# Kernel tuning notes

Measured on AMD Instinct MI355X. Metric: run time of the kernel, lower is better.

The kernel has to match this reference:

```python
import jax, jax.numpy as jnp
import numpy as np

N_BLADES = 8
D_BLADE = 128
D_FFN = 512
LN_EPS = 1e-5


def _build_cayley_signs():
    """Cl(3,0) Cayley table: blades indexed by bitmask over {e1,e2,e3}.
    signs[i, j, k] = s where blade_i * blade_j = s * blade_k (Euclidean metric)."""
    def reorder_sign(a, b):
        a >>= 1
        total = 0
        while a:
            total += bin(a & b).count('1')
            a >>= 1
        return 1.0 if total % 2 == 0 else -1.0
    signs = np.zeros((8, 8, 8), dtype=np.float32)
    for i in range(8):
        for j in range(8):
            signs[i, j, i ^ j] = reorder_sign(i, j)
    return jnp.asarray(signs)


def setup_inputs() -> dict:
    key = jax.random.key(0)
    k_x, k_g, k_u, k_d = jax.random.split(key, 4)
    B, T = 4, 4096
    x = jax.random.normal(k_x, (B, T, N_BLADES, D_BLADE), dtype=jnp.float32)
    return {
        'x': x,
        'interaction_weights': jnp.full((N_BLADES, N_BLADES), 0.1, dtype=jnp.float32),
        'geo_gate': jnp.asarray(0.5, dtype=jnp.float32),
        'ln_w': jnp.ones((D_BLADE,), dtype=jnp.float32),
        'ln_b': jnp.zeros((D_BLADE,), dtype=jnp.float32),
        'w_gate': jax.random.normal(k_g, (D_FFN, D_BLADE), dtype=jnp.float32) * 0.02,
        'w_up': jax.random.normal(k_u, (D_FFN, D_BLADE), dtype=jnp.float32) * 0.02,
        'w_down': jax.random.normal(k_d, (D_BLADE, D_FFN), dtype=jnp.float32) * 0.02,
        'cayley_signs': _build_cayley_signs(),
    }


def reference(x, interaction_weights, geo_gate, ln_w, ln_b, w_gate, w_up, w_down, cayley_signs):
    # --- full geometric self-product via Cayley table ---
    w = jax.nn.sigmoid(interaction_weights)              # (i, j)
    signed = cayley_signs * w[:, :, None]                # (i, j, k): fold weights into sign tensor
    # result[b,t,k,d] = sum_ij signed[i,j,k] * x[b,t,i,d] * x[b,t,j,d]
    geo = jnp.einsum('btid,btjd,ijk->btkd', x, x, signed)
    # --- residual gate between geometric product and input ---
    gate = jax.nn.sigmoid(geo_gate)
    mixed = gate * geo + (1.0 - gate) * x                # (B, T, N, D)
    # --- per-blade LayerNorm over d_blade ---
    mu = jnp.mean(mixed, axis=-1, keepdims=True)
    var = jnp.mean(jnp.square(mixed - mu), axis=-1, keepdims=True)
    normed = (mixed - mu) * jax.lax.rsqrt(var + LN_EPS) * ln_w + ln_b
    # --- SwiGLU FFN (no biases) ---
    g = jnp.einsum('btnd,fd->btnf', normed, w_gate)
    u = jnp.einsum('btnd,fd->btnf', normed, w_up)
    h = jax.nn.silu(g) * u
    out = jnp.einsum('btnf,df->btnd', h, w_down)
    return x + out
```

## Files before the change

### kernel.cpp

```cpp
#include <hip/hip_runtime.h>
#include <hip/hip_bf16.h>

typedef unsigned short ushort_t;
typedef __bf16 bf16_t;
typedef bf16_t bf16x8 __attribute__((ext_vector_type(8)));
typedef unsigned short u16x8v __attribute__((ext_vector_type(8)));
typedef float f32x4 __attribute__((ext_vector_type(4)));
typedef unsigned uint32x2 __attribute__((ext_vector_type(2)));
typedef unsigned uint32x4 __attribute__((ext_vector_type(4)));

#define D 128
#define NB 8
#define DFFN 512
#define LN_EPS 1e-5f

#define BARRIER_LGKM() asm volatile("s_waitcnt lgkmcnt(0)\n\ts_barrier" ::: "memory")
#define BARRIER_VM()   asm volatile("s_waitcnt vmcnt(0) lgkmcnt(0)\n\ts_barrier" ::: "memory")
#define PIN(v) asm volatile("" : "+v"(v))

__device__ __forceinline__ ushort_t bf16_rne(float f) {
  union { float f; unsigned u; } c; c.f = f;
  unsigned u = c.u;
  unsigned r = (u + 0x7FFFu + ((u >> 16) & 1u)) >> 16;
  return (ushort_t)r;
}

__device__ __forceinline__ unsigned cvt_pk_bf16(float lo, float hi) {
  unsigned r;
  asm("v_cvt_pk_bf16_f32 %0, %1, %2" : "=v"(r) : "v"(lo), "v"(hi));
  return r;
}

__device__ __forceinline__ bf16x8 loadfrag_bf(const ushort_t* p) {
  u16x8v v = *(const u16x8v*)p;
  return __builtin_bit_cast(bf16x8, v);
}

__device__ __forceinline__ bf16x8 load8_cvt(const float* p) {
  f32x4 a = *(const f32x4*)p;
  f32x4 b = *(const f32x4*)(p + 4);
  u16x8v r;
  r[0] = bf16_rne(a[0]); r[1] = bf16_rne(a[1]);
  r[2] = bf16_rne(a[2]); r[3] = bf16_rne(a[3]);
  r[4] = bf16_rne(b[0]); r[5] = bf16_rne(b[1]);
  r[6] = bf16_rne(b[2]); r[7] = bf16_rne(b[3]);
  return __builtin_bit_cast(bf16x8, r);
}

__device__ __forceinline__ f32x4 mfma16(bf16x8 a, bf16x8 b, f32x4 c) {
  return __builtin_amdgcn_mfma_f32_16x16x32_bf16(a, b, c, 0, 0, 0);
}

__device__ __forceinline__ float readlane_f(float v, int lane) {
  return __builtin_bit_cast(float, __builtin_amdgcn_readlane(__builtin_bit_cast(int, v), lane));
}

__device__ __forceinline__ float fast_rcp(float x) {
  return __builtin_amdgcn_rcpf(x);
}

typedef const __attribute__((address_space(1))) void gv_t;
typedef __attribute__((address_space(3))) void lv_t;
__device__ __forceinline__ void gload_lds16(const void* g, void* l) {
  __builtin_amdgcn_global_load_lds((gv_t*)g, (lv_t*)l, 16, 0, 0);
}

__global__ void cvt_weights(const float* __restrict__ wg,
                            const float* __restrict__ wu,
                            const float* __restrict__ wd,
                            ushort_t* __restrict__ o) {
  int i = blockIdx.x * 256 + threadIdx.x;
  const int n1 = DFFN * D;
  float v;
  if (i < n1)            v = wg[i];
  else if (i < 2 * n1)   v = wu[i - n1];
  else                   v = wd[i - 2 * n1];
  o[i] = bf16_rne(v);
}

__global__ __launch_bounds__(256)
void geo_ln(const float* __restrict__ x,
            const float* __restrict__ iw,
            const float* __restrict__ geo_gate,
            const float* __restrict__ ln_w,
            const float* __restrict__ ln_b,
            const float* __restrict__ cayley,
            ushort_t* __restrict__ Aout) {
  const int tid = threadIdx.x;
  const int w = tid >> 6;
  const int l = tid & 63;
  const int g = l >> 4;
  const int q = l & 15;

  float sgv;
  {
    int i_l = l >> 3, j_l = l & 7;
    float s = cayley[(i_l * 8 + j_l) * 8 + (i_l ^ j_l)];
    sgv = s / (1.0f + __expf(-iw[i_l * 8 + j_l]));
  }
  float cd[8], cp[28];
#pragma unroll
  for (int i = 0; i < 8; ++i) cd[i] = readlane_f(sgv, i * 8 + i);
  {
    int p = 0;
#pragma unroll
    for (int i = 0; i < 8; ++i)
#pragma unroll
      for (int j = i + 1; j < 8; ++j) { cp[p] = readlane_f(sgv, i * 8 + j) + readlane_f(sgv, j * 8 + i); ++p; }
  }
  const float gate = 1.0f / (1.0f + __expf(-geo_gate[0]));
  const float ogate = 1.0f - gate;

  const f32x4 lw0 = *(const f32x4*)(ln_w + q * 8);
  const f32x4 lw1 = *(const f32x4*)(ln_w + q * 8 + 4);
  const f32x4 lb0 = *(const f32x4*)(ln_b + q * 8);
  const f32x4 lb1 = *(const f32x4*)(ln_b + q * 8 + 4);

  const long tok = (long)blockIdx.x * 16 + w * 4 + g;
  const float* xp = x + tok * (NB * D) + q * 8;

  f32x4 xa[8], xb[8];
#pragma unroll
  for (int i = 0; i < 8; ++i) { xa[i] = *(const f32x4*)(xp + i * D); xb[i] = *(const f32x4*)(xp + i * D + 4); }

  f32x4 ga[8], gb[8];
#pragma unroll
  for (int k = 0; k < 8; ++k) { ga[k] = 0.f; gb[k] = 0.f; }
#pragma unroll
  for (int i = 0; i < 8; ++i) {
    ga[0] += cd[i] * (xa[i] * xa[i]);
    gb[0] += cd[i] * (xb[i] * xb[i]);
  }
  {
    int p = 0;
#pragma unroll
    for (int i = 0; i < 8; ++i)
#pragma unroll
      for (int j = i + 1; j < 8; ++j) {
        int k = i ^ j;
        ga[k] += cp[p] * (xa[i] * xa[j]);
        gb[k] += cp[p] * (xb[i] * xb[j]);
        ++p;
      }
  }

  ushort_t* Arow0 = Aout + tok * (8 * D);
#pragma unroll
  for (int k = 0; k < 8; ++k) {
    f32x4 m0 = gate * ga[k] + ogate * xa[k];
    f32x4 m1 = gate * gb[k] + ogate * xb[k];
    float s1 = (m0[0] + m0[1]) + (m0[2] + m0[3]) + (m1[0] + m1[1]) + (m1[2] + m1[3]);
    float s2 = m0[0]*m0[0] + m0[1]*m0[1] + m0[2]*m0[2] + m0[3]*m0[3]
             + m1[0]*m1[0] + m1[1]*m1[1] + m1[2]*m1[2] + m1[3]*m1[3];
#pragma unroll
    for (int off = 8; off; off >>= 1) {
      s1 += __shfl_xor(s1, off, 64);
      s2 += __shfl_xor(s2, off, 64);
    }
    float mu = s1 * (1.0f / 128.0f);
    float rs = rsqrtf(s2 * (1.0f / 128.0f) - mu * mu + LN_EPS);
    float nb2 = -mu * rs;
    f32x4 n0, n1;
#pragma unroll
    for (int e = 0; e < 4; ++e) {
      n0[e] = (m0[e] * rs + nb2) * lw0[e] + lb0[e];
      n1[e] = (m1[e] * rs + nb2) * lw1[e] + lb1[e];
    }
    uint32x4 pk;
    pk[0] = cvt_pk_bf16(n0[0], n0[1]);
    pk[1] = cvt_pk_bf16(n0[2], n0[3]);
    pk[2] = cvt_pk_bf16(n1[0], n1[1]);
    pk[3] = cvt_pk_bf16(n1[2], n1[3]);
    *(uint32x4*)(Arow0 + k * D + ((q ^ k) * 8)) = pk;
  }
}

__global__ __launch_bounds__(256, 3)
void ffn_mfma(const ushort_t* __restrict__ Abf,
              const float* __restrict__ x,
              const ushort_t* __restrict__ wg_bf,
              const ushort_t* __restrict__ wu_bf,
              const ushort_t* __restrict__ wd_bf,
              float* __restrict__ out) {
  __shared__ ushort_t A[64 * 128];
  __shared__ ushort_t Hb[2][64 * 64];

  const int tid = threadIdx.x;
  const int w = tid >> 6;
  const int l = tid & 63;
  const int lg = l >> 4;
  const int ln16 = l & 15;

  const long row0 = (long)blockIdx.x * 64;

  {
    const ushort_t* src = Abf + row0 * D;
#pragma unroll
    for (int i = 0; i < 4; ++i) {
      int seg = w * 4 + i;
      gload_lds16(src + seg * 512 + l * 8, &A[seg * 512]);
    }
  }

  bf16x8 bg[4], bu[4], bd[2][2];
  {
    const int frow = w * 16 + ln16;
#pragma unroll
    for (int ks = 0; ks < 4; ++ks) {
      bg[ks] = loadfrag_bf(wg_bf + frow * D + ks * 32 + lg * 8);
      bu[ks] = loadfrag_bf(wu_bf + frow * D + ks * 32 + lg * 8);
    }
#pragma unroll
    for (int nt = 0; nt < 2; ++nt) {
      int dcol = w * 32 + nt * 16 + ln16;
#pragma unroll
      for (int k2 = 0; k2 < 2; ++k2)
        bd[nt][k2] = loadfrag_bf(wd_bf + dcol * DFFN + k2 * 32 + lg * 8);
    }
  }

  BARRIER_VM();

  bf16x8 afr[4][4];
#pragma unroll
  for (int mt = 0; mt < 4; ++mt) {
    const int row = mt * 16 + ln16;
#pragma unroll
    for (int ks = 0; ks < 4; ++ks) {
      int unit = (ks * 4 + lg) ^ (row & 7);
      afr[mt][ks] = *(const bf16x8*)&A[row * 128 + unit * 8];
    }
  }
#pragma unroll
  for (int mt = 0; mt < 4; ++mt)
#pragma unroll
    for (int ks = 0; ks < 4; ++ks)
      PIN(afr[mt][ks]);

  f32x4 oacc[4][2];
#pragma unroll
  for (int mt = 0; mt < 4; ++mt)
#pragma unroll
    for (int nt = 0; nt < 2; ++nt)
#pragma unroll
      for (int r = 0; r < 4; ++r) oacc[mt][nt][r] = 0.f;

#pragma unroll
  for (int ch = 0; ch < 8; ++ch) {
    ushort_t* Hc = &Hb[ch & 1][0];

#pragma unroll
    for (int mt = 0; mt < 4; ++mt) {
      const int row = mt * 16 + ln16;
      f32x4 gacc = 0.f, uacc = 0.f;
      __builtin_amdgcn_s_setprio(1);
#pragma unroll
      for (int ks = 0; ks < 4; ++ks) {
        gacc = mfma16(bg[ks], afr[mt][ks], gacc);
        uacc = mfma16(bu[ks], afr[mt][ks], uacc);
      }
      __builtin_amdgcn_s_setprio(0);
      float h[4];
#pragma unroll
      for (int r = 0; r < 4; ++r) {
        float gv = gacc[r];
        h[r] = gv * fast_rcp(1.0f + __expf(-gv)) * uacc[r];
      }
      uint32x2 pk;
      pk[0] = cvt_pk_bf16(h[0], h[1]);
      pk[1] = cvt_pk_bf16(h[2], h[3]);
      int u = (w * 2 + (lg >> 1)) ^ (row & 7);
      *(uint32x2*)((char*)Hc + row * 128 + u * 16 + (lg & 1) * 8) = pk;
    }

    if (ch < 7) {
      const int frow = (ch + 1) * 64 + w * 16 + ln16;
#pragma unroll
      for (int ks = 0; ks < 4; ++ks) {
        bg[ks] = loadfrag_bf(wg_bf + frow * D + ks * 32 + lg * 8);
        bu[ks] = loadfrag_bf(wu_bf + frow * D + ks * 32 + lg * 8);
      }
    }

    BARRIER_LGKM();

    __builtin_amdgcn_s_setprio(1);
#pragma unroll
    for (int mt = 0; mt < 4; ++mt) {
      const int m = mt * 16 + ln16;
#pragma unroll
      for (int k2 = 0; k2 < 2; ++k2) {
        int u = (k2 * 4 + lg) ^ (m & 7);
        bf16x8 hf = *(const bf16x8*)((const char*)Hc + m * 128 + u * 16);
        oacc[mt][0] = mfma16(hf, bd[0][k2], oacc[mt][0]);
        oacc[mt][1] = mfma16(hf, bd[1][k2], oacc[mt][1]);
      }
    }
    __builtin_amdgcn_s_setprio(0);

    if (ch < 7) {
#pragma unroll
      for (int nt = 0; nt < 2; ++nt) {
        int dcol = w * 32 + nt * 16 + ln16;
#pragma unroll
        for (int k2 = 0; k2 < 2; ++k2)
          bd[nt][k2] = loadfrag_bf(wd_bf + dcol * DFFN + (ch + 1) * 64 + k2 * 32 + lg * 8);
      }
    }
  }

#pragma unroll
  for (int mt = 0; mt < 4; ++mt) {
#pragma unroll
    for (int r = 0; r < 4; ++r) {
      long rowg = row0 + mt * 16 + lg * 4 + r;
      const float* xp = x + rowg * D;
      float* op = out + rowg * D;
#pragma unroll
      for (int nt = 0; nt < 2; ++nt) {
        int d = w * 32 + nt * 16 + ln16;
        op[d] = xp[d] + oacc[mt][nt][r];
      }
    }
  }
}

template <bool WS_BF16>
__global__ __launch_bounds__(256, 2)
void fused_geo_ffn(const float* __restrict__ x,
                   const float* __restrict__ iw,
                   const float* __restrict__ geo_gate,
                   const float* __restrict__ ln_w,
                   const float* __restrict__ ln_b,
                   const float* __restrict__ w_gate_f,
                   const float* __restrict__ w_up_f,
                   const float* __restrict__ w_down_f,
                   const float* __restrict__ cayley,
                   const ushort_t* __restrict__ wg_bf,
                   const ushort_t* __restrict__ wu_bf,
                   const ushort_t* __restrict__ wd_bf,
                   float* __restrict__ out) {
  __shared__ float sg[64];
  __shared__ ushort_t A_lds[128 * 128];
  __shared__ ushort_t H_lds[128 * 64];

  const int tid = threadIdx.x;
  const int w = tid >> 6;
  const int l = tid & 63;
  const int lg = l >> 4;
  const int ln16 = l & 15;
  const int kbase = lg * 8;

  if (tid < 64) {
    int i = tid >> 3, j = tid & 7;
    float s = cayley[(i * 8 + j) * 8 + (i ^ j)];
    sg[tid] = s / (1.0f + __expf(-iw[i * 8 + j]));
  }
  __syncthreads();
  float sgr[64];
#pragma unroll
  for (int t = 0; t < 64; ++t) sgr[t] = sg[t];

  const float gate = 1.0f / (1.0f + __expf(-geo_gate[0]));
  const float2 lw = *(const float2*)(ln_w + 2 * l);
  const float2 lb = *(const float2*)(ln_b + 2 * l);
  const long tok0 = (long)blockIdx.x * 16;

  for (int tt = 0; tt < 4; ++tt) {
    int ltok = w * 4 + tt;
    const float* xp = x + (tok0 + ltok) * (long)(NB * D);
    float2 xv[8];
#pragma unroll
    for (int i = 0; i < 8; ++i) xv[i] = *(const float2*)(xp + i * D + 2 * l);
#pragma unroll
    for (int k = 0; k < 8; ++k) {
      float2 g; g.x = 0.f; g.y = 0.f;
#pragma unroll
      for (int i = 0; i < 8; ++i) {
        float s = sgr[i * 8 + (i ^ k)];
        g.x += s * xv[i].x * xv[i ^ k].x;
        g.y += s * xv[i].y * xv[i ^ k].y;
      }
      float2 m;
      m.x = gate * g.x + (1.0f - gate) * xv[k].x;
      m.y = gate * g.y + (1.0f - gate) * xv[k].y;
      float s1 = m.x + m.y;
      float s2 = m.x * m.x + m.y * m.y;
#pragma unroll
      for (int off = 32; off; off >>= 1) {
        s1 += __shfl_xor(s1, off, 64);
        s2 += __shfl_xor(s2, off, 64);
      }
      float mu = s1 * (1.0f / 128.0f);
      float rs = rsqrtf(s2 * (1.0f / 128.0f) - mu * mu + LN_EPS);
      float nx = (m.x - mu) * rs * lw.x + lb.x;
      float ny = (m.y - mu) * rs * lw.y + lb.y;
      int row = ltok * 8 + k;
      int colb = (4 * l) ^ ((row & 7) << 4);
      *(unsigned*)((char*)A_lds + row * 256 + colb) = cvt_pk_bf16(nx, ny);
    }
  }
  __syncthreads();

  f32x4 oacc[8][2];
#pragma unroll
  for (int mt = 0; mt < 8; ++mt)
#pragma unroll
    for (int nt = 0; nt < 2; ++nt)
#pragma unroll
      for (int r = 0; r < 4; ++r) oacc[mt][nt][r] = 0.f;

  for (int ch = 0; ch < 8; ++ch) {
    const int fbase = ch * 64 + w * 16 + ln16;
    bf16x8 bg[4], bu[4];
#pragma unroll
    for (int ks = 0; ks < 4; ++ks) {
      int koff = ks * 32 + kbase;
      if (WS_BF16) {
        bg[ks] = loadfrag_bf(wg_bf + fbase * D + koff);
        bu[ks] = loadfrag_bf(wu_bf + fbase * D + koff);
      } else {
        bg[ks] = load8_cvt(w_gate_f + fbase * D + koff);
        bu[ks] = load8_cvt(w_up_f + fbase * D + koff);
      }
    }
#pragma unroll
    for (int mt = 0; mt < 8; ++mt) {
      const int row = mt * 16 + ln16;
      f32x4 gacc = 0.f, uacc = 0.f;
#pragma unroll
      for (int ks = 0; ks < 4; ++ks) {
        int colb = ((ks * 32 + kbase) * 2) ^ ((row & 7) << 4);
        bf16x8 a = *(const bf16x8*)((const char*)A_lds + row * 256 + colb);
        gacc = mfma16(bg[ks], a, gacc);
        uacc = mfma16(bu[ks], a, uacc);
      }
      float h[4];
#pragma unroll
      for (int r = 0; r < 4; ++r) {
        float gv = gacc[r], uv = uacc[r];
        h[r] = gv * __builtin_amdgcn_rcpf(1.0f + __expf(-gv)) * uv;
      }
      uint32x2 pk;
      pk[0] = cvt_pk_bf16(h[0], h[1]);
      pk[1] = cvt_pk_bf16(h[2], h[3]);
      int u = (w * 2 + (lg >> 1)) ^ (row & 7);
      *(uint32x2*)&H_lds[row * 64 + u * 8 + (lg & 1) * 4] = pk;
    }
    __syncthreads();
#pragma unroll
    for (int mt = 0; mt < 8; ++mt) {
      const int row = mt * 16 + ln16;
#pragma unroll
      for (int ks = 0; ks < 2; ++ks) {
        int u = (ks * 4 + lg) ^ (row & 7);
        bf16x8 hfrag = *(const bf16x8*)&H_lds[row * 64 + u * 8];
        bf16x8 b0, b1;
        int dcol0 = w * 32 + ln16;
        int foff = ch * 64 + ks * 32 + kbase;
        if (WS_BF16) {
          b0 = loadfrag_bf(wd_bf + dcol0 * DFFN + foff);
          b1 = loadfrag_bf(wd_bf + (dcol0 + 16) * DFFN + foff);
        } else {
          b0 = load8_cvt(w_down_f + dcol0 * DFFN + foff);
          b1 = load8_cvt(w_down_f + (dcol0 + 16) * DFFN + foff);
        }
        oacc[mt][0] = mfma16(hfrag, b0, oacc[mt][0]);
        oacc[mt][1] = mfma16(hfrag, b1, oacc[mt][1]);
      }
    }
    __syncthreads();
  }

  const long rowg0 = tok0 * NB;
#pragma unroll
  for (int mt = 0; mt < 8; ++mt) {
#pragma unroll
    for (int r = 0; r < 4; ++r) {
      long row = rowg0 + mt * 16 + lg * 4 + r;
      const float* xp = x + row * D;
      float* op = out + row * D;
#pragma unroll
      for (int nt = 0; nt < 2; ++nt) {
        int d = w * 32 + nt * 16 + ln16;
        op[d] = xp[d] + oacc[mt][nt][r];
      }
    }
  }
}

extern "C" void kernel_launch(void* const* d_in, const int* in_sizes, int n_in,
                              void* d_out, int out_size, void* d_ws, size_t ws_size,
                              hipStream_t stream) {
  const float* x   = (const float*)d_in[0];
  const float* iw  = (const float*)d_in[1];
  const float* gg  = (const float*)d_in[2];
  const float* lnw = (const float*)d_in[3];
  const float* lnb = (const float*)d_in[4];
  const float* wg  = (const float*)d_in[5];
  const float* wu  = (const float*)d_in[6];
  const float* wd  = (const float*)d_in[7];
  const float* cs  = (const float*)d_in[8];
  float* out = (float*)d_out;

  const int ntok = in_sizes[0] / (NB * D);
  const int wtot = 3 * DFFN * D;
  const size_t wbytes = (size_t)wtot * 2;
  const size_t abytes = (size_t)ntok * NB * D * 2;

  if (ws_size >= wbytes + abytes) {
    ushort_t* wbf = (ushort_t*)d_ws;
    ushort_t* act = wbf + wtot;
    cvt_weights<<<wtot / 256, 256, 0, stream>>>(wg, wu, wd, wbf);
    geo_ln<<<ntok / 16, 256, 0, stream>>>(x, iw, gg, lnw, lnb, cs, act);
    ffn_mfma<<<(ntok * NB) / 64, 256, 0, stream>>>(
        act, x, wbf, wbf + DFFN * D, wbf + 2 * DFFN * D, out);
  } else if (ws_size >= wbytes) {
    ushort_t* wbf = (ushort_t*)d_ws;
    cvt_weights<<<wtot / 256, 256, 0, stream>>>(wg, wu, wd, wbf);
    fused_geo_ffn<true><<<ntok / 16, 256, 0, stream>>>(
        x, iw, gg, lnw, lnb, wg, wu, wd, cs,
        wbf, wbf + DFFN * D, wbf + 2 * DFFN * D, out);
  } else {
    fused_geo_ffn<false><<<ntok / 16, 256, 0, stream>>>(
        x, iw, gg, lnw, lnb, wg, wu, wd, cs,
        (const ushort_t*)nullptr, (const ushort_t*)nullptr, (const ushort_t*)nullptr, out);
  }
}
```

Baseline: 123.0 us.

## Fuse geometric product and LayerNorm into the MFMA FFN kernel

Folds the geo_ln stage into the FFN kernel. Each block now computes the geometric product, gating and per-blade LayerNorm for its 8 tokens and writes bf16 rows straight into LDS, instead of writing them to a global workspace and reading them back. This removes the bf16 activation round trip through HBM and one kernel launch. The cost is that the elementwise prologue, with 64-wide shuffle reductions, now runs inside the MFMA kernel and can lengthen it or limit how well it overlaps.

```diff
diff --git a/kernel.cpp b/kernel.cpp
--- a/kernel.cpp
+++ b/kernel.cpp
@@ -15,7 +15,6 @@
 #define LN_EPS 1e-5f
 
 #define BARRIER_LGKM() asm volatile("s_waitcnt lgkmcnt(0)\n\ts_barrier" ::: "memory")
-#define BARRIER_VM()   asm volatile("s_waitcnt vmcnt(0) lgkmcnt(0)\n\ts_barrier" ::: "memory")
 #define PIN(v) asm volatile("" : "+v"(v))
 
 __device__ __forceinline__ ushort_t bf16_rne(float f) {
@@ -57,12 +56,6 @@
 
 __device__ __forceinline__ float fast_rcp(float x) {
   return __builtin_amdgcn_rcpf(x);
-}
-
-typedef const __attribute__((address_space(1))) void gv_t;
-typedef __attribute__((address_space(3))) void lv_t;
-__device__ __forceinline__ void gload_lds16(const void* g, void* l) {
-  __builtin_amdgcn_global_load_lds((gv_t*)g, (lv_t*)l, 16, 0, 0);
 }
 
 __global__ void cvt_weights(const float* __restrict__ wg,
@@ -78,110 +71,17 @@
   o[i] = bf16_rne(v);
 }
 
-__global__ __launch_bounds__(256)
-void geo_ln(const float* __restrict__ x,
-            const float* __restrict__ iw,
-            const float* __restrict__ geo_gate,
-            const float* __restrict__ ln_w,
-            const float* __restrict__ ln_b,
-            const float* __restrict__ cayley,
-            ushort_t* __restrict__ Aout) {
-  const int tid = threadIdx.x;
-  const int w = tid >> 6;
-  const int l = tid & 63;
-  const int g = l >> 4;
-  const int q = l & 15;
-
-  float sgv;
-  {
-    int i_l = l >> 3, j_l = l & 7;
-    float s = cayley[(i_l * 8 + j_l) * 8 + (i_l ^ j_l)];
-    sgv = s / (1.0f + __expf(-iw[i_l * 8 + j_l]));
-  }
-  float cd[8], cp[28];
-#pragma unroll
-  for (int i = 0; i < 8; ++i) cd[i] = readlane_f(sgv, i * 8 + i);
-  {
-    int p = 0;
-#pragma unroll
-    for (int i = 0; i < 8; ++i)
-#pragma unroll
-      for (int j = i + 1; j < 8; ++j) { cp[p] = readlane_f(sgv, i * 8 + j) + readlane_f(sgv, j * 8 + i); ++p; }
-  }
-  const float gate = 1.0f / (1.0f + __expf(-geo_gate[0]));
-  const float ogate = 1.0f - gate;
-
-  const f32x4 lw0 = *(const f32x4*)(ln_w + q * 8);
-  const f32x4 lw1 = *(const f32x4*)(ln_w + q * 8 + 4);
-  const f32x4 lb0 = *(const f32x4*)(ln_b + q * 8);
-  const f32x4 lb1 = *(const f32x4*)(ln_b + q * 8 + 4);
-
-  const long tok = (long)blockIdx.x * 16 + w * 4 + g;
-  const float* xp = x + tok * (NB * D) + q * 8;
-
-  f32x4 xa[8], xb[8];
-#pragma unroll
-  for (int i = 0; i < 8; ++i) { xa[i] = *(const f32x4*)(xp + i * D); xb[i] = *(const f32x4*)(xp + i * D + 4); }
-
-  f32x4 ga[8], gb[8];
-#pragma unroll
-  for (int k = 0; k < 8; ++k) { ga[k] = 0.f; gb[k] = 0.f; }
-#pragma unroll
-  for (int i = 0; i < 8; ++i) {
-    ga[0] += cd[i] * (xa[i] * xa[i]);
-    gb[0] += cd[i] * (xb[i] * xb[i]);
-  }
-  {
-    int p = 0;
-#pragma unroll
-    for (int i = 0; i < 8; ++i)
-#pragma unroll
-      for (int j = i + 1; j < 8; ++j) {
-        int k = i ^ j;
-        ga[k] += cp[p] * (xa[i] * xa[j]);
-        gb[k] += cp[p] * (xb[i] * xb[j]);
-        ++p;
-      }
-  }
-
-  ushort_t* Arow0 = Aout + tok * (8 * D);
-#pragma unroll
-  for (int k = 0; k < 8; ++k) {
-    f32x4 m0 = gate * ga[k] + ogate * xa[k];
-    f32x4 m1 = gate * gb[k] + ogate * xb[k];
-    float s1 = (m0[0] + m0[1]) + (m0[2] + m0[3]) + (m1[0] + m1[1]) + (m1[2] + m1[3]);
-    float s2 = m0[0]*m0[0] + m0[1]*m0[1] + m0[2]*m0[2] + m0[3]*m0[3]
-             + m1[0]*m1[0] + m1[1]*m1[1] + m1[2]*m1[2] + m1[3]*m1[3];
-#pragma unroll
-    for (int off = 8; off; off >>= 1) {
-      s1 += __shfl_xor(s1, off, 64);
-      s2 += __shfl_xor(s2, off, 64);
-    }
-    float mu = s1 * (1.0f / 128.0f);
-    float rs = rsqrtf(s2 * (1.0f / 128.0f) - mu * mu + LN_EPS);
-    float nb2 = -mu * rs;
-    f32x4 n0, n1;
-#pragma unroll
-    for (int e = 0; e < 4; ++e) {
-      n0[e] = (m0[e] * rs + nb2) * lw0[e] + lb0[e];
-      n1[e] = (m1[e] * rs + nb2) * lw1[e] + lb1[e];
-    }
-    uint32x4 pk;
-    pk[0] = cvt_pk_bf16(n0[0], n0[1]);
-    pk[1] = cvt_pk_bf16(n0[2], n0[3]);
-    pk[2] = cvt_pk_bf16(n1[0], n1[1]);
-    pk[3] = cvt_pk_bf16(n1[2], n1[3]);
-    *(uint32x4*)(Arow0 + k * D + ((q ^ k) * 8)) = pk;
-  }
-}
-
 __global__ __launch_bounds__(256, 3)
-void ffn_mfma(const ushort_t* __restrict__ Abf,
-              const float* __restrict__ x,
-              const ushort_t* __restrict__ wg_bf,
-              const ushort_t* __restrict__ wu_bf,
-              const ushort_t* __restrict__ wd_bf,
-              float* __restrict__ out) {
+void geo_ffn_fused(const float* __restrict__ x,
+                   const float* __restrict__ iw,
+                   const float* __restrict__ geo_gate,
+                   const float* __restrict__ ln_w,
+                   const float* __restrict__ ln_b,
+                   const float* __restrict__ cayley,
+                   const ushort_t* __restrict__ wg_bf,
+                   const ushort_t* __restrict__ wu_bf,
+                   const ushort_t* __restrict__ wd_bf,
+                   float* __restrict__ out) {
   __shared__ ushort_t A[64 * 128];
   __shared__ ushort_t Hb[2][64 * 64];
 
@@ -191,16 +91,8 @@
   const int lg = l >> 4;
   const int ln16 = l & 15;
 
-  const long row0 = (long)blockIdx.x * 64;
-
-  {
-    const ushort_t* src = Abf + row0 * D;
-#pragma unroll
-    for (int i = 0; i < 4; ++i) {
-      int seg = w * 4 + i;
-      gload_lds16(src + seg * 512 + l * 8, &A[seg * 512]);
-    }
-  }
+  const long tok0 = (long)blockIdx.x * 8;
+  const long row0 = tok0 * NB;
 
   bf16x8 bg[4], bu[4], bd[2][2];
   {
@@ -219,7 +111,73 @@
     }
   }
 
-  BARRIER_VM();
+  float cd[8], cp[28];
+  {
+    float sgv;
+    int i_l = l >> 3, j_l = l & 7;
+    float s = cayley[(i_l * 8 + j_l) * 8 + (i_l ^ j_l)];
+    sgv = s / (1.0f + __expf(-iw[i_l * 8 + j_l]));
+#pragma unroll
+    for (int i = 0; i < 8; ++i) cd[i] = readlane_f(sgv, i * 8 + i);
+    int p = 0;
+#pragma unroll
+    for (int i = 0; i < 8; ++i)
+#pragma unroll
+      for (int j = i + 1; j < 8; ++j) { cp[p] = readlane_f(sgv, i * 8 + j) + readlane_f(sgv, j * 8 + i); ++p; }
+  }
+  const float gate = 1.0f / (1.0f + __expf(-geo_gate[0]));
+  const float ogate = 1.0f - gate;
+  const float2 lw = *(const float2*)(ln_w + 2 * l);
+  const float2 lb = *(const float2*)(ln_b + 2 * l);
+
+  for (int tt = 0; tt < 2; ++tt) {
+    const int ltok = w * 2 + tt;
+    const float* xp = x + (tok0 + ltok) * (long)(NB * D);
+    float2 xv[8];
+#pragma unroll
+    for (int i = 0; i < 8; ++i) xv[i] = *(const float2*)(xp + i * D + 2 * l);
+    float2 geo[8];
+#pragma unroll
+    for (int k = 0; k < 8; ++k) { geo[k].x = 0.f; geo[k].y = 0.f; }
+#pragma unroll
+    for (int i = 0; i < 8; ++i) {
+      geo[0].x += cd[i] * xv[i].x * xv[i].x;
+      geo[0].y += cd[i] * xv[i].y * xv[i].y;
+    }
+    {
+      int p = 0;
+#pragma unroll
+      for (int i = 0; i < 8; ++i)
+#pragma unroll
+        for (int j = i + 1; j < 8; ++j) {
+          int k = i ^ j;
+          geo[k].x += cp[p] * (xv[i].x * xv[j].x);
+          geo[k].y += cp[p] * (xv[i].y * xv[j].y);
+          ++p;
+        }
+    }
+#pragma unroll
+    for (int k = 0; k < 8; ++k) {
+      float mx = gate * geo[k].x + ogate * xv[k].x;
+      float my = gate * geo[k].y + ogate * xv[k].y;
+      float s1 = mx + my;
+      float s2 = mx * mx + my * my;
+#pragma unroll
+      for (int off = 32; off; off >>= 1) {
+        s1 += __shfl_xor(s1, off, 64);
+        s2 += __shfl_xor(s2, off, 64);
+      }
+      float mu = s1 * (1.0f / 128.0f);
+      float rs = rsqrtf(s2 * (1.0f / 128.0f) - mu * mu + LN_EPS);
+      float nx = (mx - mu) * rs * lw.x + lb.x;
+      float ny = (my - mu) * rs * lw.y + lb.y;
+      int row = ltok * 8 + k;
+      int colb = (4 * l) ^ ((row & 7) << 4);
+      *(unsigned*)((char*)A + row * 256 + colb) = cvt_pk_bf16(nx, ny);
+    }
+  }
+
+  BARRIER_LGKM();
 
   bf16x8 afr[4][4];
 #pragma unroll
@@ -325,21 +283,17 @@
   }
 }
 
-template <bool WS_BF16>
 __global__ __launch_bounds__(256, 2)
-void fused_geo_ffn(const float* __restrict__ x,
-                   const float* __restrict__ iw,
-                   const float* __restrict__ geo_gate,
-                   const float* __restrict__ ln_w,
-                   const float* __restrict__ ln_b,
-                   const float* __restrict__ w_gate_f,
-                   const float* __restrict__ w_up_f,
-                   const float* __restrict__ w_down_f,
-                   const float* __restrict__ cayley,
-                   const ushort_t* __restrict__ wg_bf,
-                   const ushort_t* __restrict__ wu_bf,
-                   const ushort_t* __restrict__ wd_bf,
-                   float* __restrict__ out) {
+void fused_geo_ffn_f32w(const float* __restrict__ x,
+                        const float* __restrict__ iw,
+                        const float* __restrict__ geo_gate,
+                        const float* __restrict__ ln_w,
+                        const float* __restrict__ ln_b,
+                        const float* __restrict__ w_gate_f,
+                        const float* __restrict__ w_up_f,
+                        const float* __restrict__ w_down_f,
+                        const float* __restrict__ cayley,
+                        float* __restrict__ out) {
   __shared__ float sg[64];
   __shared__ ushort_t A_lds[128 * 128];
   __shared__ ushort_t H_lds[128 * 64];
@@ -416,13 +370,8 @@
 #pragma unroll
     for (int ks = 0; ks < 4; ++ks) {
       int koff = ks * 32 + kbase;
-      if (WS_BF16) {
-        bg[ks] = loadfrag_bf(wg_bf + fbase * D + koff);
-        bu[ks] = loadfrag_bf(wu_bf + fbase * D + koff);
-      } else {
-        bg[ks] = load8_cvt(w_gate_f + fbase * D + koff);
-        bu[ks] = load8_cvt(w_up_f + fbase * D + koff);
-      }
+      bg[ks] = load8_cvt(w_gate_f + fbase * D + koff);
+      bu[ks] = load8_cvt(w_up_f + fbase * D + koff);
     }
 #pragma unroll
     for (int mt = 0; mt < 8; ++mt) {
@@ -455,16 +404,10 @@
       for (int ks = 0; ks < 2; ++ks) {
         int u = (ks * 4 + lg) ^ (row & 7);
         bf16x8 hfrag = *(const bf16x8*)&H_lds[row * 64 + u * 8];
-        bf16x8 b0, b1;
         int dcol0 = w * 32 + ln16;
         int foff = ch * 64 + ks * 32 + kbase;
-        if (WS_BF16) {
-          b0 = loadfrag_bf(wd_bf + dcol0 * DFFN + foff);
-          b1 = loadfrag_bf(wd_bf + (dcol0 + 16) * DFFN + foff);
-        } else {
-          b0 = load8_cvt(w_down_f + dcol0 * DFFN + foff);
-          b1 = load8_cvt(w_down_f + (dcol0 + 16) * DFFN + foff);
-        }
+        bf16x8 b0 = load8_cvt(w_down_f + dcol0 * DFFN + foff);
+        bf16x8 b1 = load8_cvt(w_down_f + (dcol0 + 16) * DFFN + foff);
         oacc[mt][0] = mfma16(hfrag, b0, oacc[mt][0]);
         oacc[mt][1] = mfma16(hfrag, b1, oacc[mt][1]);
       }
@@ -506,24 +449,15 @@
   const int ntok = in_sizes[0] / (NB * D);
   const int wtot = 3 * DFFN * D;
   const size_t wbytes = (size_t)wtot * 2;
-  const size_t abytes = (size_t)ntok * NB * D * 2;
-
-  if (ws_size >= wbytes + abytes) {
-    ushort_t* wbf = (ushort_t*)d_ws;
-    ushort_t* act = wbf + wtot;
-    cvt_weights<<<wtot / 256, 256, 0, stream>>>(wg, wu, wd, wbf);
-    geo_ln<<<ntok / 16, 256, 0, stream>>>(x, iw, gg, lnw, lnb, cs, act);
-    ffn_mfma<<<(ntok * NB) / 64, 256, 0, stream>>>(
-        act, x, wbf, wbf + DFFN * D, wbf + 2 * DFFN * D, out);
-  } else if (ws_size >= wbytes) {
+
+  if (ws_size >= wbytes) {
     ushort_t* wbf = (ushort_t*)d_ws;
     cvt_weights<<<wtot / 256, 256, 0, stream>>>(wg, wu, wd, wbf);
-    fused_geo_ffn<true><<<ntok / 16, 256, 0, stream>>>(
-        x, iw, gg, lnw, lnb, wg, wu, wd, cs,
+    geo_ffn_fused<<<ntok / 8, 256, 0, stream>>>(
+        x, iw, gg, lnw, lnb, cs,
         wbf, wbf + DFFN * D, wbf + 2 * DFFN * D, out);
   } else {
-    fused_geo_ffn<false><<<ntok / 16, 256, 0, stream>>>(
-        x, iw, gg, lnw, lnb, wg, wu, wd, cs,
-        (const ushort_t*)nullptr, (const ushort_t*)nullptr, (const ushort_t*)nullptr, out);
-  }
-}
+    fused_geo_ffn_f32w<<<ntok / 16, 256, 0, stream>>>(
+        x, iw, gg, lnw, lnb, wg, wu, wd, cs, out);
+  }
+}
```

Result: faster. 113.7 us (-7.6%).
